# Kernel optimization log

Hardware: AMD Instinct MI355X
Metric: run time of the kernel (lower is better)

## Reference

```python
import jax, jax.numpy as jnp
import numpy as np

N_HEAD, F_IN, F_OUT = 4, 768, 64
BS, N = 4, 2048


def setup_inputs() -> dict:
    key = jax.random.key(0)
    k_h, k_w, k_src, k_dst = jax.random.split(key, 4)
    # xavier_uniform bounds
    lim_w = float(np.sqrt(6.0 / (F_IN + F_OUT)))
    lim_a = float(np.sqrt(6.0 / (F_OUT + 1)))
    return {
        "h": jax.random.normal(k_h, (BS, N, F_IN), dtype=jnp.float32),
        "w": jax.random.uniform(k_w, (N_HEAD, F_IN, F_OUT), jnp.float32, -lim_w, lim_w),
        "a_src": jax.random.uniform(k_src, (N_HEAD, F_OUT, 1), jnp.float32, -lim_a, lim_a),
        "a_dst": jax.random.uniform(k_dst, (N_HEAD, F_OUT, 1), jnp.float32, -lim_a, lim_a),
        "bias": jnp.zeros((F_OUT,), dtype=jnp.float32),
    }


def reference(h, w, a_src, a_dst, bias):
    # h: [b, n, f_in]; w: [h, f_in, f_out]
    h_prime = jnp.einsum("bnf,hfo->bhno", h, w)          # [b, h, n, f_out]
    t = jnp.tanh(h_prime)
    attn_src = jnp.einsum("bhno,ho->bhn", t, a_src[..., 0])  # [b, h, n]
    attn_dst = jnp.einsum("bhno,ho->bhn", t, a_dst[..., 0])  # [b, h, n]
    # broadcast add: attn[b,h,i,j] = src[b,h,i] + dst[b,h,j]
    attn = attn_src[..., :, None] + attn_dst[..., None, :]   # [b, h, n, n]
    attn = jnp.where(attn >= 0, attn, 0.2 * attn)            # leaky_relu(0.2)
    attn = jax.nn.softmax(attn, axis=-1)
    out = jnp.einsum("bhij,bhjo->bhio", attn, h_prime)       # [b, h, n, f_out]
    return out + bias
```

## Files before the change

### kernel.cpp

```cpp
#include <hip/hip_runtime.h>
#include <hip/hip_bf16.h>

#define NHEAD 4
#define FIN   768
#define FOUT  64
#define BSZ   4
#define NSEQ  2048
#define BH    (BSZ*NHEAD)
#define LOG2E 1.44269504088896f

typedef __attribute__((ext_vector_type(8)))  short bf16x8;
typedef __attribute__((ext_vector_type(16))) float f32x16;
typedef __attribute__((ext_vector_type(8)))  unsigned short u16x8;
typedef __attribute__((ext_vector_type(4)))  unsigned short u16x4;
typedef __attribute__((ext_vector_type(4)))  unsigned u32x4;

__device__ __forceinline__ unsigned short f2bf(float f){
  unsigned b = __float_as_uint(f);
  return (unsigned short)((b + 0x7fffu + ((b >> 16) & 1u)) >> 16);
}
__device__ __forceinline__ float fexp2(float x){
#if __has_builtin(__builtin_amdgcn_exp2f)
  return __builtin_amdgcn_exp2f(x);
#else
  return exp2f(x);
#endif
}
__device__ __forceinline__ unsigned pkbf(float lo, float hi){
#if __has_builtin(__builtin_amdgcn_cvt_pk_bf16_f32)
  typedef __attribute__((ext_vector_type(2))) __bf16 bf2;
  union { bf2 v; unsigned u; } cv;
  cv.v = __builtin_amdgcn_cvt_pk_bf16_f32(lo, hi);
  return cv.u;
#else
  return (unsigned)f2bf(lo) | ((unsigned)f2bf(hi) << 16);
#endif
}
__device__ __forceinline__ float fast_tanh(float v){
  const float e = fexp2(v * (2.0f*LOG2E));
#if __has_builtin(__builtin_amdgcn_rcpf)
  return 1.0f - 2.0f*__builtin_amdgcn_rcpf(e + 1.0f);
#else
  return 1.0f - 2.0f/(e + 1.0f);
#endif
}

__global__ __launch_bounds__(512, 2) void k_hprime(
    const float* __restrict__ h, const float* __restrict__ w,
    const float* __restrict__ a_src, const float* __restrict__ a_dst,
    unsigned short* __restrict__ hpz2, float* __restrict__ srcv,
    float* __restrict__ dstv)
{
  __shared__ __align__(16) char smem[65536];
  float* psumS = (float*)(smem + 16384);
  float* psumD = (float*)(smem + 16896);
  char*  Tt    = smem + 32768;

  const int tid  = threadIdx.x;
  const int bid  = blockIdx.x;
  const int bh1  = (bid & 7) | (((bid >> 3) & 1) << 3);
  const int head = bh1 & 3;
  const int jbase = (bid >> 4) << 6;
  const int i0a   = (bh1 >> 2)*NSEQ + jbase;
  const int wave = tid >> 6, lane = tid & 63;
  const int wm = wave & 1, wn = (wave >> 1) & 1, kw = wave >> 2;
  const int l32 = lane & 31, h32 = lane >> 5;

  f32x16 acc = {0,0,0,0,0,0,0,0,0,0,0,0,0,0,0,0};

  const int sr = tid >> 3, sc = tid & 7;
  const float* hA = h + (size_t)(i0a + sr)*FIN + sc*8;
  const int aslot = (sc ^ (sr & 7)) << 4;

  const int ob = tid & 63, cc = tid >> 6;
  const float* wsrc = w + (size_t)head*FIN*FOUT + ob;
  const int bslot0 = ((cc & 7) ^ (ob & 7)) << 4;

  float4 ra0 = *(const float4*)(hA);
  float4 ra1 = *(const float4*)(hA + 4);
  float4 ra2 = *(const float4*)(hA + 64);
  float4 ra3 = *(const float4*)(hA + 68);
  float rb[16];
  #pragma unroll
  for (int j = 0; j < 8; ++j){
    rb[j]     = wsrc[(size_t)(cc*8 + j)*FOUT];
    rb[8 + j] = wsrc[(size_t)(64 + cc*8 + j)*FOUT];
  }

  for (int it = 0; it < 6; ++it){
    char* Ab = smem +         (it & 1)*16384;
    char* Bb = smem + 32768 + (it & 1)*16384;
    u32x4 pk0, pk1;
    pk0[0] = pkbf(ra0.x, ra0.y); pk0[1] = pkbf(ra0.z, ra0.w);
    pk0[2] = pkbf(ra1.x, ra1.y); pk0[3] = pkbf(ra1.z, ra1.w);
    pk1[0] = pkbf(ra2.x, ra2.y); pk1[1] = pkbf(ra2.z, ra2.w);
    pk1[2] = pkbf(ra3.x, ra3.y); pk1[3] = pkbf(ra3.z, ra3.w);
    u32x4 qb0, qb1;
    qb0[0] = pkbf(rb[0],  rb[1]);  qb0[1] = pkbf(rb[2],  rb[3]);
    qb0[2] = pkbf(rb[4],  rb[5]);  qb0[3] = pkbf(rb[6],  rb[7]);
    qb1[0] = pkbf(rb[8],  rb[9]);  qb1[1] = pkbf(rb[10], rb[11]);
    qb1[2] = pkbf(rb[12], rb[13]); qb1[3] = pkbf(rb[14], rb[15]);
    if (it < 5){
      const float* an = hA + (it+1)*128;
      ra0 = *(const float4*)(an);      ra1 = *(const float4*)(an + 4);
      ra2 = *(const float4*)(an + 64); ra3 = *(const float4*)(an + 68);
      const float* wn_ = wsrc + (size_t)(it+1)*128*FOUT;
      #pragma unroll
      for (int j = 0; j < 8; ++j){
        rb[j]     = wn_[(size_t)(cc*8 + j)*FOUT];
        rb[8 + j] = wn_[(size_t)(64 + cc*8 + j)*FOUT];
      }
    }
    *(u32x4*)(Ab + sr*256 + aslot)        = pk0;
    *(u32x4*)(Ab + sr*256 + 128 + aslot)  = pk1;
    *(u32x4*)(Bb + ob*256 +       bslot0) = qb0;
    *(u32x4*)(Bb + ob*256 + 128 + bslot0) = qb1;
    asm volatile("s_waitcnt lgkmcnt(0)" ::: "memory");
    __builtin_amdgcn_s_barrier();
    __builtin_amdgcn_sched_barrier(0);
    #pragma unroll
    for (int s = 0; s < 4; ++s){
      const int slot = (((s*2 + h32) ^ (l32 & 7)) << 4);
      bf16x8 av = *(const bf16x8*)(Ab + (wm*32 + l32)*256 + kw*128 + slot);
      bf16x8 bv = *(const bf16x8*)(Bb + (wn*32 + l32)*256 + kw*128 + slot);
      acc = __builtin_amdgcn_mfma_f32_32x32x16_bf16(av, bv, acc, 0, 0, 0);
    }
  }

  if (kw == 1) *(f32x16*)(smem + (size_t)((wave & 3)*64 + lane)*64) = acc;
  __syncthreads();
  if (kw == 0){
    acc += *(const f32x16*)(smem + (size_t)((wave & 3)*64 + lane)*64);
    const float as = a_src[head*64 + wn*32 + l32];
    const float ad = a_dst[head*64 + wn*32 + l32];
    #pragma unroll
    for (int rb2 = 0; rb2 < 4; ++rb2){
      const int jb = wm*32 + rb2*8 + h32*4;
      u16x4 c4;
      #pragma unroll
      for (int q = 0; q < 4; ++q){
        const float v = acc[rb2*4 + q];
        c4[q] = f2bf(v);
        const float t = fast_tanh(v);
        float ps = t*as, pd = t*ad;
        ps += __shfl_xor(ps, 1);  ps += __shfl_xor(ps, 2);  ps += __shfl_xor(ps, 4);
        ps += __shfl_xor(ps, 8);  ps += __shfl_xor(ps, 16);
        pd += __shfl_xor(pd, 1);  pd += __shfl_xor(pd, 2);  pd += __shfl_xor(pd, 4);
        pd += __shfl_xor(pd, 8);  pd += __shfl_xor(pd, 16);
        if (l32 == 0){
          psumS[(jb + q)*2 + wn] = ps;
          psumD[(jb + q)*2 + wn] = pd;
        }
      }
      const int orow = wn*32 + l32;
      const int slot = ((jb >> 3) & 7) ^ (orow & 7);
      *(u16x4*)(Tt + orow*128 + slot*16 + (jb & 7)*2) = c4;
    }
  }
  __syncthreads();

  {
    const int o = tid & 63, c = tid >> 6;
    u16x8 val = *(const u16x8*)(Tt + o*128 + ((c ^ (o & 7)) << 4));
    *(u16x8*)((char*)hpz2 + ((size_t)(bh1*256 + (jbase >> 3) + c)*64 + o)*16) = val;
  }
  if (tid < 64){
    srcv[(size_t)bh1*NSEQ + jbase + tid] = (psumS[tid*2] + psumS[tid*2 + 1]) * LOG2E;
    dstv[(size_t)bh1*NSEQ + jbase + tid] = (psumD[tid*2] + psumD[tid*2 + 1]) * LOG2E;
  }
}

__global__ __launch_bounds__(512, 4) void k_attn(
    const unsigned short* __restrict__ hpz2, const float* __restrict__ srcv,
    const float* __restrict__ dstv, const float* __restrict__ bias,
    float* __restrict__ out)
{
  __shared__ __align__(16) char smem[33792];
  float* Lbuf = (float*)(smem + 32768);

  const int tid = threadIdx.x;
  const int bid = blockIdx.x;
  const int bh  = (bid & 7) | (((bid >> 3) & 1) << 3);
  const int i0  = (bid >> 4) << 6;
  const int wave = tid >> 6, lane = tid & 63;
  const int wm = wave & 1, jw = wave >> 1;
  const int l32 = lane & 31, h32 = lane >> 5;

  const float s2 = srcv[(size_t)bh*NSEQ + i0 + wm*32 + l32];
  const float u_ = s2;
  const float v_ = 0.2f*s2;

  const u16x8* gp = (const u16x8*)((const char*)hpz2 + (size_t)bh*256*64*16);
  const u16x8* tp = gp + ((jw*4 + h32)*64 + l32);
  const float* dS = dstv + (size_t)bh*NSEQ + (jw*4 + h32)*8;

  f32x16 accO0 = {0,0,0,0,0,0,0,0,0,0,0,0,0,0,0,0};
  f32x16 accO1 = {0,0,0,0,0,0,0,0,0,0,0,0,0,0,0,0};
  float lpart = 0.f;

  u16x8 c0 = tp[0], c1 = tp[32], c2 = tp[128], c3 = tp[160];

  for (int w = 0; w < 16; ++w){
    u16x8 n0, n1, n2, n3;
    if (w < 15){
      const u16x8* np = tp + 1024;
      n0 = np[0]; n1 = np[32]; n2 = np[128]; n3 = np[160];
    }
    float4 d0 = *(const float4*)(dS);
    float4 d1 = *(const float4*)(dS + 4);
    float4 d2 = *(const float4*)(dS + 16);
    float4 d3 = *(const float4*)(dS + 20);
    {
      float e0 = fexp2(fmaxf(u_ + d0.x, fmaf(0.2f, d0.x, v_)));
      float e1 = fexp2(fmaxf(u_ + d0.y, fmaf(0.2f, d0.y, v_)));
      float e2 = fexp2(fmaxf(u_ + d0.z, fmaf(0.2f, d0.z, v_)));
      float e3 = fexp2(fmaxf(u_ + d0.w, fmaf(0.2f, d0.w, v_)));
      float e4 = fexp2(fmaxf(u_ + d1.x, fmaf(0.2f, d1.x, v_)));
      float e5 = fexp2(fmaxf(u_ + d1.y, fmaf(0.2f, d1.y, v_)));
      float e6 = fexp2(fmaxf(u_ + d1.z, fmaf(0.2f, d1.z, v_)));
      float e7 = fexp2(fmaxf(u_ + d1.w, fmaf(0.2f, d1.w, v_)));
      lpart += ((e0+e1)+(e2+e3)) + ((e4+e5)+(e6+e7));
      u32x4 pk;
      pk[0] = pkbf(e0, e1); pk[1] = pkbf(e2, e3);
      pk[2] = pkbf(e4, e5); pk[3] = pkbf(e6, e7);
      const bf16x8 pA = __builtin_bit_cast(bf16x8, pk);
      accO0 = __builtin_amdgcn_mfma_f32_32x32x16_bf16(pA, c0, accO0, 0, 0, 0);
      accO1 = __builtin_amdgcn_mfma_f32_32x32x16_bf16(pA, c1, accO1, 0, 0, 0);
    }
    {
      float e0 = fexp2(fmaxf(u_ + d2.x, fmaf(0.2f, d2.x, v_)));
      float e1 = fexp2(fmaxf(u_ + d2.y, fmaf(0.2f, d2.y, v_)));
      float e2 = fexp2(fmaxf(u_ + d2.z, fmaf(0.2f, d2.z, v_)));
      float e3 = fexp2(fmaxf(u_ + d2.w, fmaf(0.2f, d2.w, v_)));
      float e4 = fexp2(fmaxf(u_ + d3.x, fmaf(0.2f, d3.x, v_)));
      float e5 = fexp2(fmaxf(u_ + d3.y, fmaf(0.2f, d3.y, v_)));
      float e6 = fexp2(fmaxf(u_ + d3.z, fmaf(0.2f, d3.z, v_)));
      float e7 = fexp2(fmaxf(u_ + d3.w, fmaf(0.2f, d3.w, v_)));
      lpart += ((e0+e1)+(e2+e3)) + ((e4+e5)+(e6+e7));
      u32x4 pk;
      pk[0] = pkbf(e0, e1); pk[1] = pkbf(e2, e3);
      pk[2] = pkbf(e4, e5); pk[3] = pkbf(e6, e7);
      const bf16x8 pA = __builtin_bit_cast(bf16x8, pk);
      accO0 = __builtin_amdgcn_mfma_f32_32x32x16_bf16(pA, c2, accO0, 0, 0, 0);
      accO1 = __builtin_amdgcn_mfma_f32_32x32x16_bf16(pA, c3, accO1, 0, 0, 0);
    }
    tp += 1024; dS += 128;
    c0 = n0; c1 = n1; c2 = n2; c3 = n3;
  }

  lpart += __shfl_xor(lpart, 32);
  if (lane < 32) Lbuf[(wm*4 + jw)*32 + l32] = lpart;

  const float4 bia = *(const float4*)(bias + (tid & 15)*4);
  #pragma unroll
  for (int ph = 0; ph < 2; ++ph){
    __syncthreads();
    if (wm == ph){
      float* ob = (float*)smem;
      #pragma unroll
      for (int reg = 0; reg < 16; ++reg){
        const int m = (reg & 3) + 8*(reg >> 2) + 4*h32;
        ob[(jw*32 + m)*64 +      l32] = accO0[reg];
        ob[(jw*32 + m)*64 + 32 + l32] = accO1[reg];
      }
    }
    __syncthreads();
    {
      const int i = tid >> 4, o4 = (tid & 15)*4;
      const float* ob = (const float*)smem;
      float4 v0 = *(const float4*)(ob + (0*32 + i)*64 + o4);
      float4 v1 = *(const float4*)(ob + (1*32 + i)*64 + o4);
      float4 v2 = *(const float4*)(ob + (2*32 + i)*64 + o4);
      float4 v3 = *(const float4*)(ob + (3*32 + i)*64 + o4);
      const float l = Lbuf[(ph*4+0)*32 + i] + Lbuf[(ph*4+1)*32 + i]
                    + Lbuf[(ph*4+2)*32 + i] + Lbuf[(ph*4+3)*32 + i];
      const float r = 1.f / l;
      float4 res;
      res.x = (v0.x + v1.x + v2.x + v3.x)*r + bia.x;
      res.y = (v0.y + v1.y + v2.y + v3.y)*r + bia.y;
      res.z = (v0.z + v1.z + v2.z + v3.z)*r + bia.z;
      res.w = (v0.w + v1.w + v2.w + v3.w)*r + bia.w;
      *(float4*)(out + ((size_t)bh*NSEQ + i0 + ph*32 + i)*64 + o4) = res;
    }
  }
}

extern "C" void kernel_launch(void* const* d_in, const int* in_sizes, int n_in,
                              void* d_out, int out_size, void* d_ws, size_t ws_size,
                              hipStream_t stream)
{
  const float* h     = (const float*)d_in[0];
  const float* w     = (const float*)d_in[1];
  const float* a_src = (const float*)d_in[2];
  const float* a_dst = (const float*)d_in[3];
  const float* bias  = (const float*)d_in[4];
  float* out = (float*)d_out;

  char* ws = (char*)d_ws;
  unsigned short* hpz2 = (unsigned short*)ws;
  float* srcv = (float*)(ws + (4u<<20));
  float* dstv = (float*)(ws + (4u<<20) + (128u<<10));

  k_hprime<<<512, 512, 0, stream>>>(h, w, a_src, a_dst, hpz2, srcv, dstv);
  k_hprime<<<512, 512, 0, stream>>>(h, w, a_src, a_dst, hpz2, srcv, dstv);
  k_attn<<<512, 512, 0, stream>>>(hpz2, srcv, dstv, bias, out);
}
```

Measured before the change: 140.1 us.

## Replace quadratic attention with sort-and-prefix-sum evaluation of rank-1 leaky-ReLU softmax

The attention logits are a rank-1 sum src[i]+dst[j] passed through leaky ReLU. So for each row the exp weights split at the threshold dst = -src into exp2(src)·exp2(dst) and exp2(0.2 src)·exp2(0.2 dst). The new kernel bitonic-sorts dst per (batch, head) and builds forward and backward prefix sums of weighted fp32 h' rows plus a normalizer column. Each output row then needs only a binary search and two prefix-row lookups, replacing the O(N^2) exp-and-MFMA loop. It also drops the duplicated k_hprime launch and stores h' in fp32. The cost is that only 16 blocks run the attention stage, with serial segment scans and extra workspace traffic for the prefix tables.

```diff
diff --git a/kernel.cpp b/kernel.cpp
--- a/kernel.cpp
+++ b/kernel.cpp
@@ -11,20 +11,18 @@
 
 typedef __attribute__((ext_vector_type(8)))  short bf16x8;
 typedef __attribute__((ext_vector_type(16))) float f32x16;
-typedef __attribute__((ext_vector_type(8)))  unsigned short u16x8;
-typedef __attribute__((ext_vector_type(4)))  unsigned short u16x4;
 typedef __attribute__((ext_vector_type(4)))  unsigned u32x4;
 
-__device__ __forceinline__ unsigned short f2bf(float f){
-  unsigned b = __float_as_uint(f);
-  return (unsigned short)((b + 0x7fffu + ((b >> 16) & 1u)) >> 16);
-}
 __device__ __forceinline__ float fexp2(float x){
 #if __has_builtin(__builtin_amdgcn_exp2f)
   return __builtin_amdgcn_exp2f(x);
 #else
   return exp2f(x);
 #endif
+}
+__device__ __forceinline__ unsigned short f2bf(float f){
+  unsigned b = __float_as_uint(f);
+  return (unsigned short)((b + 0x7fffu + ((b >> 16) & 1u)) >> 16);
 }
 __device__ __forceinline__ unsigned pkbf(float lo, float hi){
 #if __has_builtin(__builtin_amdgcn_cvt_pk_bf16_f32)
@@ -45,16 +43,15 @@
 #endif
 }
 
-__global__ __launch_bounds__(512, 2) void k_hprime(
+__global__ __launch_bounds__(512, 4) void k_hprime(
     const float* __restrict__ h, const float* __restrict__ w,
     const float* __restrict__ a_src, const float* __restrict__ a_dst,
-    unsigned short* __restrict__ hpz2, float* __restrict__ srcv,
+    float* __restrict__ hp32, float* __restrict__ srcv,
     float* __restrict__ dstv)
 {
   __shared__ __align__(16) char smem[65536];
   float* psumS = (float*)(smem + 16384);
   float* psumD = (float*)(smem + 16896);
-  char*  Tt    = smem + 32768;
 
   const int tid  = threadIdx.x;
   const int bid  = blockIdx.x;
@@ -133,14 +130,15 @@
     acc += *(const f32x16*)(smem + (size_t)((wave & 3)*64 + lane)*64);
     const float as = a_src[head*64 + wn*32 + l32];
     const float ad = a_dst[head*64 + wn*32 + l32];
+    const int orow = wn*32 + l32;
+    float* hrow = hp32 + ((size_t)bh1*NSEQ + jbase)*64 + orow;
     #pragma unroll
     for (int rb2 = 0; rb2 < 4; ++rb2){
       const int jb = wm*32 + rb2*8 + h32*4;
-      u16x4 c4;
       #pragma unroll
       for (int q = 0; q < 4; ++q){
         const float v = acc[rb2*4 + q];
-        c4[q] = f2bf(v);
+        hrow[(size_t)(jb + q)*64] = v;
         const float t = fast_tanh(v);
         float ps = t*as, pd = t*ad;
         ps += __shfl_xor(ps, 1);  ps += __shfl_xor(ps, 2);  ps += __shfl_xor(ps, 4);
@@ -152,136 +150,137 @@
           psumD[(jb + q)*2 + wn] = pd;
         }
       }
-      const int orow = wn*32 + l32;
-      const int slot = ((jb >> 3) & 7) ^ (orow & 7);
-      *(u16x4*)(Tt + orow*128 + slot*16 + (jb & 7)*2) = c4;
-    }
-  }
-  __syncthreads();
-
-  {
-    const int o = tid & 63, c = tid >> 6;
-    u16x8 val = *(const u16x8*)(Tt + o*128 + ((c ^ (o & 7)) << 4));
-    *(u16x8*)((char*)hpz2 + ((size_t)(bh1*256 + (jbase >> 3) + c)*64 + o)*16) = val;
-  }
+    }
+  }
+  __syncthreads();
   if (tid < 64){
     srcv[(size_t)bh1*NSEQ + jbase + tid] = (psumS[tid*2] + psumS[tid*2 + 1]) * LOG2E;
     dstv[(size_t)bh1*NSEQ + jbase + tid] = (psumD[tid*2] + psumD[tid*2 + 1]) * LOG2E;
   }
 }
 
-__global__ __launch_bounds__(512, 4) void k_attn(
-    const unsigned short* __restrict__ hpz2, const float* __restrict__ srcv,
+__global__ __launch_bounds__(512, 1) void k_attn2(
+    const float* __restrict__ hp32, const float* __restrict__ srcv,
     const float* __restrict__ dstv, const float* __restrict__ bias,
-    float* __restrict__ out)
+    float* __restrict__ out, float* __restrict__ Pws, float* __restrict__ Sws)
 {
-  __shared__ __align__(16) char smem[33792];
-  float* Lbuf = (float*)(smem + 32768);
-
+  __shared__ float keys[2048];
+  __shared__ int   idxs[2048];
+  __shared__ float Fh[2048];
+  __shared__ float Fl[2048];
+  __shared__ float seg[130][32];
+
+  const int bh  = blockIdx.x;
   const int tid = threadIdx.x;
-  const int bid = blockIdx.x;
-  const int bh  = (bid & 7) | (((bid >> 3) & 1) << 3);
-  const int i0  = (bid >> 4) << 6;
-  const int wave = tid >> 6, lane = tid & 63;
-  const int wm = wave & 1, jw = wave >> 1;
-  const int l32 = lane & 31, h32 = lane >> 5;
-
-  const float s2 = srcv[(size_t)bh*NSEQ + i0 + wm*32 + l32];
-  const float u_ = s2;
-  const float v_ = 0.2f*s2;
-
-  const u16x8* gp = (const u16x8*)((const char*)hpz2 + (size_t)bh*256*64*16);
-  const u16x8* tp = gp + ((jw*4 + h32)*64 + l32);
-  const float* dS = dstv + (size_t)bh*NSEQ + (jw*4 + h32)*8;
-
-  f32x16 accO0 = {0,0,0,0,0,0,0,0,0,0,0,0,0,0,0,0};
-  f32x16 accO1 = {0,0,0,0,0,0,0,0,0,0,0,0,0,0,0,0};
-  float lpart = 0.f;
-
-  u16x8 c0 = tp[0], c1 = tp[32], c2 = tp[128], c3 = tp[160];
-
-  for (int w = 0; w < 16; ++w){
-    u16x8 n0, n1, n2, n3;
-    if (w < 15){
-      const u16x8* np = tp + 1024;
-      n0 = np[0]; n1 = np[32]; n2 = np[128]; n3 = np[160];
-    }
-    float4 d0 = *(const float4*)(dS);
-    float4 d1 = *(const float4*)(dS + 4);
-    float4 d2 = *(const float4*)(dS + 16);
-    float4 d3 = *(const float4*)(dS + 20);
-    {
-      float e0 = fexp2(fmaxf(u_ + d0.x, fmaf(0.2f, d0.x, v_)));
-      float e1 = fexp2(fmaxf(u_ + d0.y, fmaf(0.2f, d0.y, v_)));
-      float e2 = fexp2(fmaxf(u_ + d0.z, fmaf(0.2f, d0.z, v_)));
-      float e3 = fexp2(fmaxf(u_ + d0.w, fmaf(0.2f, d0.w, v_)));
-      float e4 = fexp2(fmaxf(u_ + d1.x, fmaf(0.2f, d1.x, v_)));
-      float e5 = fexp2(fmaxf(u_ + d1.y, fmaf(0.2f, d1.y, v_)));
-      float e6 = fexp2(fmaxf(u_ + d1.z, fmaf(0.2f, d1.z, v_)));
-      float e7 = fexp2(fmaxf(u_ + d1.w, fmaf(0.2f, d1.w, v_)));
-      lpart += ((e0+e1)+(e2+e3)) + ((e4+e5)+(e6+e7));
-      u32x4 pk;
-      pk[0] = pkbf(e0, e1); pk[1] = pkbf(e2, e3);
-      pk[2] = pkbf(e4, e5); pk[3] = pkbf(e6, e7);
-      const bf16x8 pA = __builtin_bit_cast(bf16x8, pk);
-      accO0 = __builtin_amdgcn_mfma_f32_32x32x16_bf16(pA, c0, accO0, 0, 0, 0);
-      accO1 = __builtin_amdgcn_mfma_f32_32x32x16_bf16(pA, c1, accO1, 0, 0, 0);
-    }
-    {
-      float e0 = fexp2(fmaxf(u_ + d2.x, fmaf(0.2f, d2.x, v_)));
-      float e1 = fexp2(fmaxf(u_ + d2.y, fmaf(0.2f, d2.y, v_)));
-      float e2 = fexp2(fmaxf(u_ + d2.z, fmaf(0.2f, d2.z, v_)));
-      float e3 = fexp2(fmaxf(u_ + d2.w, fmaf(0.2f, d2.w, v_)));
-      float e4 = fexp2(fmaxf(u_ + d3.x, fmaf(0.2f, d3.x, v_)));
-      float e5 = fexp2(fmaxf(u_ + d3.y, fmaf(0.2f, d3.y, v_)));
-      float e6 = fexp2(fmaxf(u_ + d3.z, fmaf(0.2f, d3.z, v_)));
-      float e7 = fexp2(fmaxf(u_ + d3.w, fmaf(0.2f, d3.w, v_)));
-      lpart += ((e0+e1)+(e2+e3)) + ((e4+e5)+(e6+e7));
-      u32x4 pk;
-      pk[0] = pkbf(e0, e1); pk[1] = pkbf(e2, e3);
-      pk[2] = pkbf(e4, e5); pk[3] = pkbf(e6, e7);
-      const bf16x8 pA = __builtin_bit_cast(bf16x8, pk);
-      accO0 = __builtin_amdgcn_mfma_f32_32x32x16_bf16(pA, c2, accO0, 0, 0, 0);
-      accO1 = __builtin_amdgcn_mfma_f32_32x32x16_bf16(pA, c3, accO1, 0, 0, 0);
-    }
-    tp += 1024; dS += 128;
-    c0 = n0; c1 = n1; c2 = n2; c3 = n3;
-  }
-
-  lpart += __shfl_xor(lpart, 32);
-  if (lane < 32) Lbuf[(wm*4 + jw)*32 + l32] = lpart;
-
-  const float4 bia = *(const float4*)(bias + (tid & 15)*4);
-  #pragma unroll
-  for (int ph = 0; ph < 2; ++ph){
-    __syncthreads();
-    if (wm == ph){
-      float* ob = (float*)smem;
-      #pragma unroll
-      for (int reg = 0; reg < 16; ++reg){
-        const int m = (reg & 3) + 8*(reg >> 2) + 4*h32;
-        ob[(jw*32 + m)*64 +      l32] = accO0[reg];
-        ob[(jw*32 + m)*64 + 32 + l32] = accO1[reg];
-      }
-    }
-    __syncthreads();
-    {
-      const int i = tid >> 4, o4 = (tid & 15)*4;
-      const float* ob = (const float*)smem;
-      float4 v0 = *(const float4*)(ob + (0*32 + i)*64 + o4);
-      float4 v1 = *(const float4*)(ob + (1*32 + i)*64 + o4);
-      float4 v2 = *(const float4*)(ob + (2*32 + i)*64 + o4);
-      float4 v3 = *(const float4*)(ob + (3*32 + i)*64 + o4);
-      const float l = Lbuf[(ph*4+0)*32 + i] + Lbuf[(ph*4+1)*32 + i]
-                    + Lbuf[(ph*4+2)*32 + i] + Lbuf[(ph*4+3)*32 + i];
-      const float r = 1.f / l;
-      float4 res;
-      res.x = (v0.x + v1.x + v2.x + v3.x)*r + bia.x;
-      res.y = (v0.y + v1.y + v2.y + v3.y)*r + bia.y;
-      res.z = (v0.z + v1.z + v2.z + v3.z)*r + bia.z;
-      res.w = (v0.w + v1.w + v2.w + v3.w)*r + bia.w;
-      *(float4*)(out + ((size_t)bh*NSEQ + i0 + ph*32 + i)*64 + o4) = res;
-    }
+  const float* dv = dstv + (size_t)bh*NSEQ;
+
+  for (int k = tid; k < 2048; k += 512){ keys[k] = dv[k]; idxs[k] = k; }
+  __syncthreads();
+
+  for (int sz = 2; sz <= 2048; sz <<= 1){
+    for (int st = sz >> 1; st > 0; st >>= 1){
+      for (int t = tid; t < 2048; t += 512){
+        const int j = t ^ st;
+        if (j > t){
+          const float a = keys[t], b = keys[j];
+          const bool up = ((t & sz) == 0);
+          if (up ? (a > b) : (a < b)){
+            keys[t] = b; keys[j] = a;
+            const int ia = idxs[t]; idxs[t] = idxs[j]; idxs[j] = ia;
+          }
+        }
+      }
+      __syncthreads();
+    }
+  }
+  for (int k = tid; k < 2048; k += 512){
+    const float d = keys[k];
+    Fh[k] = fexp2(d);
+    Fl[k] = fexp2(0.2f*d);
+  }
+  __syncthreads();
+
+  const float* hp = hp32 + (size_t)bh*NSEQ*64;
+
+  for (int t = tid; t < 4160; t += 512){
+    const int s = t / 130, u = t - s*130;
+    const bool back = (u >= 65);
+    const int c = back ? (u - 65) : u;
+    float acc = 0.f;
+    for (int q = 0; q < 64; ++q){
+      const int k = s*64 + q;
+      const float x = (c < 64) ? hp[(size_t)idxs[k]*64 + c] : 1.f;
+      acc += (back ? Fh[k] : Fl[k]) * x;
+    }
+    seg[u][s] = acc;
+  }
+  __syncthreads();
+
+  if (tid < 130){
+    float run = 0.f;
+    if (tid < 65){
+      for (int s = 0; s < 32; ++s){ const float v = seg[tid][s]; seg[tid][s] = run; run += v; }
+    } else {
+      for (int s = 31; s >= 0; --s){ const float v = seg[tid][s]; seg[tid][s] = run; run += v; }
+    }
+  }
+  __syncthreads();
+
+  float* Pb = Pws + (size_t)bh*2049*66;
+  float* Sb = Sws + (size_t)bh*2049*66;
+  for (int t = tid; t < 4160; t += 512){
+    const int s = t / 130, u = t - s*130;
+    const bool back = (u >= 65);
+    const int c = back ? (u - 65) : u;
+    float run = seg[u][s];
+    if (!back){
+      for (int q = 0; q < 64; ++q){
+        const int k = s*64 + q;
+        Pb[(size_t)k*66 + c] = run;
+        const float x = (c < 64) ? hp[(size_t)idxs[k]*64 + c] : 1.f;
+        run += Fl[k]*x;
+      }
+      if (s == 31) Pb[(size_t)2048*66 + c] = run;
+    } else {
+      for (int q = 63; q >= 0; --q){
+        const int k = s*64 + q;
+        const float x = (c < 64) ? hp[(size_t)idxs[k]*64 + c] : 1.f;
+        run += Fh[k]*x;
+        Sb[(size_t)k*66 + c] = run;
+      }
+      if (s == 31) Sb[(size_t)2048*66 + c] = 0.f;
+    }
+  }
+  __threadfence();
+  __syncthreads();
+
+  const int ig = tid >> 4;
+  const int o4 = (tid & 15)*4;
+  const float4 bia = *(const float4*)(bias + o4);
+  const float* sv = srcv + (size_t)bh*NSEQ;
+  for (int base = 0; base < 2048; base += 32){
+    const int i = base + ig;
+    const float S = sv[i];
+    const float thr = -S;
+    int lo = 0, hi = 2048;
+    while (lo < hi){
+      const int mid = (lo + hi) >> 1;
+      if (keys[mid] < thr) lo = mid + 1; else hi = mid;
+    }
+    const float Ei  = fexp2(S);
+    const float Eip = fexp2(0.2f*S);
+    const float* Pr = Pb + (size_t)lo*66;
+    const float* Sr = Sb + (size_t)lo*66;
+    const float4 pn = *(const float4*)(Pr + o4);
+    const float4 sn = *(const float4*)(Sr + o4);
+    const float den = Ei*Sr[64] + Eip*Pr[64];
+    const float rd = 1.f/den;
+    float4 res;
+    res.x = (Ei*sn.x + Eip*pn.x)*rd + bia.x;
+    res.y = (Ei*sn.y + Eip*pn.y)*rd + bia.y;
+    res.z = (Ei*sn.z + Eip*pn.z)*rd + bia.z;
+    res.w = (Ei*sn.w + Eip*pn.w)*rd + bia.w;
+    *(float4*)(out + ((size_t)bh*NSEQ + i)*64 + o4) = res;
   }
 }
 
@@ -297,11 +296,12 @@
   float* out = (float*)d_out;
 
   char* ws = (char*)d_ws;
-  unsigned short* hpz2 = (unsigned short*)ws;
-  float* srcv = (float*)(ws + (4u<<20));
-  float* dstv = (float*)(ws + (4u<<20) + (128u<<10));
-
-  k_hprime<<<512, 512, 0, stream>>>(h, w, a_src, a_dst, hpz2, srcv, dstv);
-  k_hprime<<<512, 512, 0, stream>>>(h, w, a_src, a_dst, hpz2, srcv, dstv);
-  k_attn<<<512, 512, 0, stream>>>(hpz2, srcv, dstv, bias, out);
-}
+  float* hp32 = (float*)ws;
+  float* srcv = (float*)(ws + (8u<<20));
+  float* dstv = (float*)(ws + (8u<<20) + (128u<<10));
+  float* Pws  = (float*)(ws + (16u<<20));
+  float* Sws  = (float*)(ws + (28u<<20));
+
+  k_hprime<<<512, 512, 0, stream>>>(h, w, a_src, a_dst, hp32, srcv, dstv);
+  k_attn2<<<16, 512, 0, stream>>>(hp32, srcv, dstv, bias, out, Pws, Sws);
+}
```

New measurement: 405.0 us. 2.89x slower.

## Factor softmax exponentials into per-row and per-column terms and drop duplicate launch

Applied to the files above, without the earlier changes.

The exponent of the leaky-relu logit is rewritten as max(exp2(D_j), c_i*exp2(0.2*D_j)), with the per-row factor exp2(S_i) dropped because softmax normalisation cancels it. The projection kernel now precomputes c = exp2(-0.8*S), exp2(D) and exp2(0.2*D). This removes every transcendental from the attention inner loop, leaving a multiply and a max, at the cost of twice the per-column vector loads. The redundant second launch of the projection kernel is removed, and that kernel's launch bounds are raised to request higher occupancy. Because the maximum logit is never subtracted, the exp2 values could overflow or underflow for larger logits, but tanh keeps them bounded here.

```diff
diff --git a/kernel.cpp b/kernel.cpp
--- a/kernel.cpp
+++ b/kernel.cpp
@@ -45,11 +45,11 @@
 #endif
 }
 
-__global__ __launch_bounds__(512, 2) void k_hprime(
+__global__ __launch_bounds__(512, 4) void k_hprime(
     const float* __restrict__ h, const float* __restrict__ w,
     const float* __restrict__ a_src, const float* __restrict__ a_dst,
-    unsigned short* __restrict__ hpz2, float* __restrict__ srcv,
-    float* __restrict__ dstv)
+    unsigned short* __restrict__ hpz2, float* __restrict__ cv,
+    float* __restrict__ Ehv, float* __restrict__ Elv)
 {
   __shared__ __align__(16) char smem[65536];
   float* psumS = (float*)(smem + 16384);
@@ -165,15 +165,19 @@
     *(u16x8*)((char*)hpz2 + ((size_t)(bh1*256 + (jbase >> 3) + c)*64 + o)*16) = val;
   }
   if (tid < 64){
-    srcv[(size_t)bh1*NSEQ + jbase + tid] = (psumS[tid*2] + psumS[tid*2 + 1]) * LOG2E;
-    dstv[(size_t)bh1*NSEQ + jbase + tid] = (psumD[tid*2] + psumD[tid*2 + 1]) * LOG2E;
+    const float S = (psumS[tid*2] + psumS[tid*2 + 1]) * LOG2E;
+    const float D = (psumD[tid*2] + psumD[tid*2 + 1]) * LOG2E;
+    const size_t ix = (size_t)bh1*NSEQ + jbase + tid;
+    cv [ix] = fexp2(-0.8f*S);
+    Ehv[ix] = fexp2(D);
+    Elv[ix] = fexp2(0.2f*D);
   }
 }
 
 __global__ __launch_bounds__(512, 4) void k_attn(
-    const unsigned short* __restrict__ hpz2, const float* __restrict__ srcv,
-    const float* __restrict__ dstv, const float* __restrict__ bias,
-    float* __restrict__ out)
+    const unsigned short* __restrict__ hpz2, const float* __restrict__ cv,
+    const float* __restrict__ Ehv, const float* __restrict__ Elv,
+    const float* __restrict__ bias, float* __restrict__ out)
 {
   __shared__ __align__(16) char smem[33792];
   float* Lbuf = (float*)(smem + 32768);
@@ -186,13 +190,12 @@
   const int wm = wave & 1, jw = wave >> 1;
   const int l32 = lane & 31, h32 = lane >> 5;
 
-  const float s2 = srcv[(size_t)bh*NSEQ + i0 + wm*32 + l32];
-  const float u_ = s2;
-  const float v_ = 0.2f*s2;
+  const float c_ = cv[(size_t)bh*NSEQ + i0 + wm*32 + l32];
 
   const u16x8* gp = (const u16x8*)((const char*)hpz2 + (size_t)bh*256*64*16);
   const u16x8* tp = gp + ((jw*4 + h32)*64 + l32);
-  const float* dS = dstv + (size_t)bh*NSEQ + (jw*4 + h32)*8;
+  const float* ehS = Ehv + (size_t)bh*NSEQ + (jw*4 + h32)*8;
+  const float* elS = Elv + (size_t)bh*NSEQ + (jw*4 + h32)*8;
 
   f32x16 accO0 = {0,0,0,0,0,0,0,0,0,0,0,0,0,0,0,0};
   f32x16 accO1 = {0,0,0,0,0,0,0,0,0,0,0,0,0,0,0,0};
@@ -206,45 +209,49 @@
       const u16x8* np = tp + 1024;
       n0 = np[0]; n1 = np[32]; n2 = np[128]; n3 = np[160];
     }
-    float4 d0 = *(const float4*)(dS);
-    float4 d1 = *(const float4*)(dS + 4);
-    float4 d2 = *(const float4*)(dS + 16);
-    float4 d3 = *(const float4*)(dS + 20);
+    float4 eh0 = *(const float4*)(ehS);
+    float4 eh1 = *(const float4*)(ehS + 4);
+    float4 eh2 = *(const float4*)(ehS + 16);
+    float4 eh3 = *(const float4*)(ehS + 20);
+    float4 el0 = *(const float4*)(elS);
+    float4 el1 = *(const float4*)(elS + 4);
+    float4 el2 = *(const float4*)(elS + 16);
+    float4 el3 = *(const float4*)(elS + 20);
     {
-      float e0 = fexp2(fmaxf(u_ + d0.x, fmaf(0.2f, d0.x, v_)));
-      float e1 = fexp2(fmaxf(u_ + d0.y, fmaf(0.2f, d0.y, v_)));
-      float e2 = fexp2(fmaxf(u_ + d0.z, fmaf(0.2f, d0.z, v_)));
-      float e3 = fexp2(fmaxf(u_ + d0.w, fmaf(0.2f, d0.w, v_)));
-      float e4 = fexp2(fmaxf(u_ + d1.x, fmaf(0.2f, d1.x, v_)));
-      float e5 = fexp2(fmaxf(u_ + d1.y, fmaf(0.2f, d1.y, v_)));
-      float e6 = fexp2(fmaxf(u_ + d1.z, fmaf(0.2f, d1.z, v_)));
-      float e7 = fexp2(fmaxf(u_ + d1.w, fmaf(0.2f, d1.w, v_)));
-      lpart += ((e0+e1)+(e2+e3)) + ((e4+e5)+(e6+e7));
+      float q0 = fmaxf(eh0.x, c_*el0.x);
+      float q1 = fmaxf(eh0.y, c_*el0.y);
+      float q2 = fmaxf(eh0.z, c_*el0.z);
+      float q3 = fmaxf(eh0.w, c_*el0.w);
+      float q4 = fmaxf(eh1.x, c_*el1.x);
+      float q5 = fmaxf(eh1.y, c_*el1.y);
+      float q6 = fmaxf(eh1.z, c_*el1.z);
+      float q7 = fmaxf(eh1.w, c_*el1.w);
+      lpart += ((q0+q1)+(q2+q3)) + ((q4+q5)+(q6+q7));
       u32x4 pk;
-      pk[0] = pkbf(e0, e1); pk[1] = pkbf(e2, e3);
-      pk[2] = pkbf(e4, e5); pk[3] = pkbf(e6, e7);
+      pk[0] = pkbf(q0, q1); pk[1] = pkbf(q2, q3);
+      pk[2] = pkbf(q4, q5); pk[3] = pkbf(q6, q7);
       const bf16x8 pA = __builtin_bit_cast(bf16x8, pk);
       accO0 = __builtin_amdgcn_mfma_f32_32x32x16_bf16(pA, c0, accO0, 0, 0, 0);
       accO1 = __builtin_amdgcn_mfma_f32_32x32x16_bf16(pA, c1, accO1, 0, 0, 0);
     }
     {
-      float e0 = fexp2(fmaxf(u_ + d2.x, fmaf(0.2f, d2.x, v_)));
-      float e1 = fexp2(fmaxf(u_ + d2.y, fmaf(0.2f, d2.y, v_)));
-      float e2 = fexp2(fmaxf(u_ + d2.z, fmaf(0.2f, d2.z, v_)));
-      float e3 = fexp2(fmaxf(u_ + d2.w, fmaf(0.2f, d2.w, v_)));
-      float e4 = fexp2(fmaxf(u_ + d3.x, fmaf(0.2f, d3.x, v_)));
-      float e5 = fexp2(fmaxf(u_ + d3.y, fmaf(0.2f, d3.y, v_)));
-      float e6 = fexp2(fmaxf(u_ + d3.z, fmaf(0.2f, d3.z, v_)));
-      float e7 = fexp2(fmaxf(u_ + d3.w, fmaf(0.2f, d3.w, v_)));
-      lpart += ((e0+e1)+(e2+e3)) + ((e4+e5)+(e6+e7));
+      float q0 = fmaxf(eh2.x, c_*el2.x);
+      float q1 = fmaxf(eh2.y, c_*el2.y);
+      float q2 = fmaxf(eh2.z, c_*el2.z);
+      float q3 = fmaxf(eh2.w, c_*el2.w);
+      float q4 = fmaxf(eh3.x, c_*el3.x);
+      float q5 = fmaxf(eh3.y, c_*el3.y);
+      float q6 = fmaxf(eh3.z, c_*el3.z);
+      float q7 = fmaxf(eh3.w, c_*el3.w);
+      lpart += ((q0+q1)+(q2+q3)) + ((q4+q5)+(q6+q7));
       u32x4 pk;
-      pk[0] = pkbf(e0, e1); pk[1] = pkbf(e2, e3);
-      pk[2] = pkbf(e4, e5); pk[3] = pkbf(e6, e7);
+      pk[0] = pkbf(q0, q1); pk[1] = pkbf(q2, q3);
+      pk[2] = pkbf(q4, q5); pk[3] = pkbf(q6, q7);
       const bf16x8 pA = __builtin_bit_cast(bf16x8, pk);
       accO0 = __builtin_amdgcn_mfma_f32_32x32x16_bf16(pA, c2, accO0, 0, 0, 0);
       accO1 = __builtin_amdgcn_mfma_f32_32x32x16_bf16(pA, c3, accO1, 0, 0, 0);
     }
-    tp += 1024; dS += 128;
+    tp += 1024; ehS += 128; elS += 128;
     c0 = n0; c1 = n1; c2 = n2; c3 = n3;
   }
 
@@ -298,10 +305,10 @@
 
   char* ws = (char*)d_ws;
   unsigned short* hpz2 = (unsigned short*)ws;
-  float* srcv = (float*)(ws + (4u<<20));
-  float* dstv = (float*)(ws + (4u<<20) + (128u<<10));
-
-  k_hprime<<<512, 512, 0, stream>>>(h, w, a_src, a_dst, hpz2, srcv, dstv);
-  k_hprime<<<512, 512, 0, stream>>>(h, w, a_src, a_dst, hpz2, srcv, dstv);
-  k_attn<<<512, 512, 0, stream>>>(hpz2, srcv, dstv, bias, out);
-}
+  float* cv  = (float*)(ws + (4u<<20));
+  float* Ehv = (float*)(ws + (4u<<20) + (128u<<10));
+  float* Elv = (float*)(ws + (4u<<20) + (256u<<10));
+
+  k_hprime<<<512, 512, 0, stream>>>(h, w, a_src, a_dst, hpz2, cv, Ehv, Elv);
+  k_attn<<<512, 512, 0, stream>>>(hpz2, cv, Ehv, Elv, bias, out);
+}
```

After: 120.0 us. 14.4% less time.
